# Kernel tuning notes

Measured on AMD Instinct MI355X. Metric: run time of the kernel, lower is better.

The kernel has to match this reference:

```python
import jax, jax.numpy as jnp
import numpy as np

B, H, N, D = 2, 16, 2048, 128

def setup_inputs() -> dict:
    key = jax.random.key(0)
    kq, kk, kv = jax.random.split(key, 3)
    q = jax.random.normal(kq, (B, H, N, D), dtype=jnp.float32)
    k = jax.random.normal(kk, (B, H, N, D), dtype=jnp.float32)
    v = jax.random.normal(kv, (B, H, N, D), dtype=jnp.float32)
    return {"q": q, "k": k, "v": v}

def reference(q, k, v):
    # scale = 1/sqrt(d) computed at forward time (scale=None in __init__)
    d = q.shape[-1]
    scale = 1.0 / jnp.sqrt(jnp.asarray(d, dtype=q.dtype))
    # scores: (B, H, N, N)
    scores = jnp.einsum('bhnd,bhmd->bhnm', q, k) * scale
    probs = jax.nn.softmax(scores, axis=-1)
    return jnp.einsum('bhnm,bhmd->bhnd', probs, v)
```

## Files before the change

kernel.cpp:

```cpp
#include <hip/hip_runtime.h>
#include <hip/hip_bf16.h>
#include <stdint.h>

#define BATCH 2
#define HEADS 16
#define BH    32
#define SEQ   2048
#define DIM   128
#define ELEMS (BATCH*HEADS*SEQ*DIM)

#define KVB   64
#define NT    (SEQ/KVB)

using f32x4  = __attribute__((ext_vector_type(4))) float;
using f32x16 = __attribute__((ext_vector_type(16))) float;
using bf16x8 = __attribute__((ext_vector_type(8))) short;
using us4    = __attribute__((ext_vector_type(4))) unsigned short;

__device__ __forceinline__ unsigned short f2bf(float f) {
    union { float f; uint32_t u; } v; v.f = f;
    uint32_t u = v.u;
    uint32_t r = u + 0x7FFFu + ((u >> 16) & 1u);
    return (unsigned short)(r >> 16);
}

__device__ __forceinline__ uint32_t packbf2(float lo, float hi) {
    __hip_bfloat162 h2 = __float22bfloat162_rn(make_float2(lo, hi));
    union { __hip_bfloat162 h; uint32_t u; } c; c.h = h2;
    return c.u;
}

__global__ __launch_bounds__(256) void prep(const float* __restrict__ K,
                                            const float* __restrict__ V,
                                            unsigned short* __restrict__ kb,
                                            unsigned short* __restrict__ vt) {
    const int b = blockIdx.x, t = threadIdx.x;
    if (b < 2048) {
        size_t base = (size_t)b * 4096 + t * 4;
        #pragma unroll
        for (int j = 0; j < 4; ++j) {
            f32x4 v = *(const f32x4*)(K + base + j * 1024);
            us4 o;
            #pragma unroll
            for (int jj = 0; jj < 4; ++jj) o[jj] = f2bf(v[jj]);
            *(us4*)(kb + base + j * 1024) = o;
        }
    } else {
        __shared__ unsigned short tile[64][66];
        const int b2 = b - 2048;
        const int bh = b2 >> 6, rem = b2 & 63;
        const int n0 = (rem >> 1) * 64, d0 = (rem & 1) * 64;
        const int rr = t >> 4, cc = t & 15;
        #pragma unroll
        for (int j = 0; j < 4; ++j) {
            int row = rr + 16 * j;
            f32x4 v = *(const f32x4*)(V + ((size_t)bh * SEQ + n0 + row) * DIM + d0 + cc * 4);
            #pragma unroll
            for (int jj = 0; jj < 4; ++jj) tile[row][cc * 4 + jj] = f2bf(v[jj]);
        }
        __syncthreads();
        #pragma unroll
        for (int j = 0; j < 4; ++j) {
            int drow = rr + 16 * j;
            us4 o;
            #pragma unroll
            for (int jj = 0; jj < 4; ++jj) o[jj] = tile[cc * 4 + jj][drow];
            *(us4*)(vt + ((size_t)bh * DIM + d0 + drow) * SEQ + n0 + cc * 4) = o;
        }
    }
}

__global__ __launch_bounds__(256, 2) void attn_fwd(const float* __restrict__ Qf,
                                                   const unsigned short* __restrict__ Kb,
                                                   const unsigned short* __restrict__ VTb,
                                                   float* __restrict__ Out) {
    __shared__ __attribute__((aligned(16))) char smem[65536];

    const int head = blockIdx.y;
    const int wid  = threadIdx.x >> 6;
    const int lane = threadIdx.x & 63;
    const int l31  = lane & 31;
    const int hL   = lane >> 5;
    const int q0   = blockIdx.x * 128 + wid * 32;

    const char* KhB  = (const char*)(Kb  + (size_t)head * SEQ * DIM);
    const char* VThB = (const char*)(VTb + (size_t)head * DIM * SEQ);

    const float scl = 0.08838834764831845f * 1.4426950408889634f;
    bf16x8 qf[8];
    {
        const float* qrow = Qf + ((size_t)head * SEQ + q0 + l31) * DIM + 8 * hL;
        #pragma unroll
        for (int u = 0; u < 8; ++u) {
            f32x4 a = *(const f32x4*)(qrow + 16 * u);
            f32x4 b = *(const f32x4*)(qrow + 16 * u + 4);
            union { uint32_t w[4]; bf16x8 v; } P;
            P.w[0] = packbf2(a[0] * scl, a[1] * scl);
            P.w[1] = packbf2(a[2] * scl, a[3] * scl);
            P.w[2] = packbf2(b[0] * scl, b[1] * scl);
            P.w[3] = packbf2(b[2] * scl, b[3] * scl);
            qf[u] = P.v;
        }
    }

    f32x16 acc[4];
    #pragma unroll
    for (int m = 0; m < 4; ++m) acc[m] = (f32x16)(0.f);
    float m_run = -INFINITY, l_run = 0.f;

    const int swzK = (l31 & 15) << 4;
    const int swzV = ((l31 >> 1) & 7) << 4;

    auto STAGE = [&](int buf, int kv0) {
        #pragma unroll
        for (int i = 0; i < 4; ++i) {
            int seg = wid * 4 + i;
            int r   = seg * 4 + (lane >> 4);
            int cb  = ((lane & 15) << 4) ^ ((r & 15) << 4);
            const char* g = KhB + (((size_t)(kv0 + r)) << 8) + cb;
            __builtin_amdgcn_global_load_lds(
                (const __attribute__((address_space(1))) void*)g,
                (__attribute__((address_space(3))) void*)(smem + buf * 16384 + seg * 1024),
                16, 0, 0);
        }
        #pragma unroll
        for (int i = 0; i < 4; ++i) {
            int seg = wid * 4 + i;
            int rp  = seg * 4 + (lane >> 4);
            int q8  = (lane & 15) << 4;
            int pre = q8 ^ ((rp & 7) << 4);
            int r   = 2 * rp + (pre >> 7);
            int cb  = pre & 127;
            const char* g = VThB + (size_t)r * (SEQ * 2) + ((size_t)kv0 << 1) + cb;
            __builtin_amdgcn_global_load_lds(
                (const __attribute__((address_space(1))) void*)g,
                (__attribute__((address_space(3))) void*)(smem + 32768 + buf * 16384 + seg * 1024),
                16, 0, 0);
        }
    };

    STAGE(0, 0);

    for (int t = 0; t < NT; ++t) {
        const int cur = t & 1;
        if (t + 1 < NT) {
            STAGE(cur ^ 1, (t + 1) * KVB);
            asm volatile("s_waitcnt vmcnt(8)" ::: "memory");
        } else {
            asm volatile("s_waitcnt vmcnt(0)" ::: "memory");
        }
        __builtin_amdgcn_s_barrier();
        asm volatile("" ::: "memory");

        const char* kb = smem + cur * 16384;
        const char* vb = smem + 32768 + cur * 16384;

        f32x16 s0 = (f32x16)(0.f), s1 = (f32x16)(0.f);
        __builtin_amdgcn_s_setprio(1);
        {
            const char* krow0 = kb + (size_t)l31 * 256;
            const char* krow1 = kb + (size_t)(32 + l31) * 256;
            #pragma unroll
            for (int u = 0; u < 8; ++u) {
                int cb = (32 * u + 16 * hL) ^ swzK;
                bf16x8 k0 = *(const bf16x8*)(krow0 + cb);
                bf16x8 k1 = *(const bf16x8*)(krow1 + cb);
                s0 = __builtin_amdgcn_mfma_f32_32x32x16_bf16(k0, qf[u], s0, 0, 0, 0);
                s1 = __builtin_amdgcn_mfma_f32_32x32x16_bf16(k1, qf[u], s1, 0, 0, 0);
            }
        }
        __builtin_amdgcn_s_setprio(0);

        bf16x8 vf[2][2][4];
        #pragma unroll
        for (int tt = 0; tt < 2; ++tt)
            #pragma unroll
            for (int ssi = 0; ssi < 2; ++ssi) {
                const int cbv = (32 * (2 * tt + ssi) + 16 * hL) + ((l31 & 1) << 7);
                #pragma unroll
                for (int m = 0; m < 4; ++m) {
                    int rp = 16 * m + (l31 >> 1);
                    vf[tt][ssi][m] = *(const bf16x8*)(vb + (size_t)rp * 256 + (cbv ^ swzV));
                }
            }

        float smax = -1e30f;
        #pragma unroll
        for (int r = 0; r < 16; ++r)
            smax = fmaxf(smax, fmaxf(s0[r], s1[r]));
        smax = fmaxf(smax, __shfl_xor(smax, 16) * 0.f + __shfl_xor(smax, 32));
        if (!__all(smax - m_run <= 8.f)) {
            float mnew = fmaxf(m_run, smax);
            float corr = __builtin_amdgcn_exp2f(m_run - mnew);
            #pragma unroll
            for (int m = 0; m < 4; ++m) acc[m] *= corr;
            l_run *= corr;
            m_run = mnew;
        }

        float psum = 0.f;
        #pragma unroll
        for (int r = 0; r < 16; ++r) {
            s0[r] = __builtin_amdgcn_exp2f(s0[r] - m_run);
            s1[r] = __builtin_amdgcn_exp2f(s1[r] - m_run);
            psum += s0[r] + s1[r];
        }
        l_run += psum;

        uint32_t w0[8], w1[8];
        #pragma unroll
        for (int k2 = 0; k2 < 8; ++k2) {
            w0[k2] = packbf2(s0[2 * k2], s0[2 * k2 + 1]);
            w1[k2] = packbf2(s1[2 * k2], s1[2 * k2 + 1]);
        }

        __builtin_amdgcn_s_setprio(1);
        #pragma unroll
        for (int tt = 0; tt < 2; ++tt) {
            #pragma unroll
            for (int ssi = 0; ssi < 2; ++ssi) {
                uint32_t A0 = tt ? w1[4 * ssi]     : w0[4 * ssi];
                uint32_t A1 = tt ? w1[4 * ssi + 1] : w0[4 * ssi + 1];
                uint32_t C0 = tt ? w1[4 * ssi + 2] : w0[4 * ssi + 2];
                uint32_t C1 = tt ? w1[4 * ssi + 3] : w0[4 * ssi + 3];
                uint32_t o0 = hL ? A0 : C0;
                uint32_t o1 = hL ? A1 : C1;
                uint32_t e0 = (uint32_t)__shfl_xor((int)o0, 32);
                uint32_t e1 = (uint32_t)__shfl_xor((int)o1, 32);
                union { uint32_t u[4]; bf16x8 v; } Bf;
                Bf.u[0] = hL ? e0 : A0;
                Bf.u[1] = hL ? e1 : A1;
                Bf.u[2] = hL ? C0 : e0;
                Bf.u[3] = hL ? C1 : e1;
                #pragma unroll
                for (int m = 0; m < 4; ++m)
                    acc[m] = __builtin_amdgcn_mfma_f32_32x32x16_bf16(vf[tt][ssi][m], Bf.v, acc[m], 0, 0, 0);
            }
        }
        __builtin_amdgcn_s_setprio(0);

        asm volatile("" ::: "memory");
        __builtin_amdgcn_s_barrier();
    }

    __syncthreads();
    const float l_tot = l_run + __shfl_xor(l_run, 32);
    const float inv = 1.0f / l_tot;
    float* ob = (float*)(smem + wid * 16384);
    #pragma unroll
    for (int m = 0; m < 4; ++m) {
        #pragma unroll
        for (int r = 0; r < 16; ++r) {
            int d = 32 * m + (r & 3) + 8 * (r >> 2) + 4 * hL;
            ob[l31 * 128 + (d ^ ((l31 & 7) << 2))] = acc[m][r] * inv;
        }
    }
    __syncthreads();
    {
        float* outp = Out + ((size_t)head * SEQ + q0) * DIM;
        #pragma unroll
        for (int i = 0; i < 16; ++i) {
            int row = 2 * i + hL;
            f32x4 v = *(const f32x4*)(ob + row * 128 + ((4 * l31) ^ ((row & 7) << 2)));
            *(f32x4*)(outp + (size_t)row * DIM + 4 * l31) = v;
        }
    }
}

extern "C" void kernel_launch(void* const* d_in, const int* in_sizes, int n_in,
                              void* d_out, int out_size, void* d_ws, size_t ws_size,
                              hipStream_t stream) {
    (void)in_sizes; (void)n_in; (void)out_size;
    const float* q = (const float*)d_in[0];
    const float* k = (const float*)d_in[1];
    const float* v = (const float*)d_in[2];
    float* out = (float*)d_out;

    const size_t needed = (size_t)ELEMS * 2 * 2;
    if (ws_size < needed) return;

    unsigned short* kb = (unsigned short*)d_ws;
    unsigned short* vt = kb + ELEMS;

    prep<<<4096, 256, 0, stream>>>(k, v, kb, vt);
    attn_fwd<<<dim3(SEQ / 128, BH), 256, 0, stream>>>(q, kb, vt, out);
}
```

Measured before the change: 220.0 us.

## Pre-convert scaled Q to bf16 in prep kernel and load V fragments lazily

Q scaling and bf16 conversion move out of the attention kernel into the prep kernel, so attn_fwd loads bf16 Q directly and prep launches 2048 more blocks. V fragment LDS loads move from a batch before the softmax to right before each PV MFMA, which lowers register pressure but may expose LDS latency. A redundant shuffle in the row-max reduction is also dropped. The extra Q write and re-read through global memory adds traffic in exchange for less fp32 Q traffic in the main kernel.

```diff
diff --git a/kernel.cpp b/kernel.cpp
--- a/kernel.cpp
+++ b/kernel.cpp
@@ -30,24 +30,31 @@
     return c.u;
 }
 
-__global__ __launch_bounds__(256) void prep(const float* __restrict__ K,
+__global__ __launch_bounds__(256) void prep(const float* __restrict__ Q,
+                                            const float* __restrict__ K,
                                             const float* __restrict__ V,
+                                            unsigned short* __restrict__ qb,
                                             unsigned short* __restrict__ kb,
                                             unsigned short* __restrict__ vt) {
     const int b = blockIdx.x, t = threadIdx.x;
-    if (b < 2048) {
-        size_t base = (size_t)b * 4096 + t * 4;
+    const float scl = 0.08838834764831845f * 1.4426950408889634f;
+    if (b < 4096) {
+        const bool isQ = b < 2048;
+        const float* src = isQ ? Q : K;
+        unsigned short* dst = isQ ? qb : kb;
+        const float f = isQ ? scl : 1.0f;
+        size_t base = (size_t)(isQ ? b : b - 2048) * 4096 + t * 4;
         #pragma unroll
         for (int j = 0; j < 4; ++j) {
-            f32x4 v = *(const f32x4*)(K + base + j * 1024);
+            f32x4 v = *(const f32x4*)(src + base + j * 1024);
             us4 o;
             #pragma unroll
-            for (int jj = 0; jj < 4; ++jj) o[jj] = f2bf(v[jj]);
-            *(us4*)(kb + base + j * 1024) = o;
+            for (int jj = 0; jj < 4; ++jj) o[jj] = f2bf(v[jj] * f);
+            *(us4*)(dst + base + j * 1024) = o;
         }
     } else {
         __shared__ unsigned short tile[64][66];
-        const int b2 = b - 2048;
+        const int b2 = b - 4096;
         const int bh = b2 >> 6, rem = b2 & 63;
         const int n0 = (rem >> 1) * 64, d0 = (rem & 1) * 64;
         const int rr = t >> 4, cc = t & 15;
@@ -70,7 +77,7 @@
     }
 }
 
-__global__ __launch_bounds__(256, 2) void attn_fwd(const float* __restrict__ Qf,
+__global__ __launch_bounds__(256, 2) void attn_fwd(const unsigned short* __restrict__ Qb,
                                                    const unsigned short* __restrict__ Kb,
                                                    const unsigned short* __restrict__ VTb,
                                                    float* __restrict__ Out) {
@@ -83,24 +90,15 @@
     const int hL   = lane >> 5;
     const int q0   = blockIdx.x * 128 + wid * 32;
 
+    const unsigned short* Qh = Qb + (size_t)head * SEQ * DIM;
     const char* KhB  = (const char*)(Kb  + (size_t)head * SEQ * DIM);
     const char* VThB = (const char*)(VTb + (size_t)head * DIM * SEQ);
 
-    const float scl = 0.08838834764831845f * 1.4426950408889634f;
     bf16x8 qf[8];
     {
-        const float* qrow = Qf + ((size_t)head * SEQ + q0 + l31) * DIM + 8 * hL;
-        #pragma unroll
-        for (int u = 0; u < 8; ++u) {
-            f32x4 a = *(const f32x4*)(qrow + 16 * u);
-            f32x4 b = *(const f32x4*)(qrow + 16 * u + 4);
-            union { uint32_t w[4]; bf16x8 v; } P;
-            P.w[0] = packbf2(a[0] * scl, a[1] * scl);
-            P.w[1] = packbf2(a[2] * scl, a[3] * scl);
-            P.w[2] = packbf2(b[0] * scl, b[1] * scl);
-            P.w[3] = packbf2(b[2] * scl, b[3] * scl);
-            qf[u] = P.v;
-        }
+        const char* qrow = (const char*)(Qh + (size_t)(q0 + l31) * DIM) + 16 * hL;
+        #pragma unroll
+        for (int u = 0; u < 8; ++u) qf[u] = *(const bf16x8*)(qrow + 32 * u);
     }
 
     f32x16 acc[4];
@@ -171,24 +169,12 @@
         }
         __builtin_amdgcn_s_setprio(0);
 
-        bf16x8 vf[2][2][4];
-        #pragma unroll
-        for (int tt = 0; tt < 2; ++tt)
-            #pragma unroll
-            for (int ssi = 0; ssi < 2; ++ssi) {
-                const int cbv = (32 * (2 * tt + ssi) + 16 * hL) + ((l31 & 1) << 7);
-                #pragma unroll
-                for (int m = 0; m < 4; ++m) {
-                    int rp = 16 * m + (l31 >> 1);
-                    vf[tt][ssi][m] = *(const bf16x8*)(vb + (size_t)rp * 256 + (cbv ^ swzV));
-                }
-            }
-
         float smax = -1e30f;
         #pragma unroll
         for (int r = 0; r < 16; ++r)
             smax = fmaxf(smax, fmaxf(s0[r], s1[r]));
-        smax = fmaxf(smax, __shfl_xor(smax, 16) * 0.f + __shfl_xor(smax, 32));
+        smax = fmaxf(smax, __shfl_xor(smax, 32));
+
         if (!__all(smax - m_run <= 8.f)) {
             float mnew = fmaxf(m_run, smax);
             float corr = __builtin_amdgcn_exp2f(m_run - mnew);
@@ -232,9 +218,13 @@
                 Bf.u[1] = hL ? e1 : A1;
                 Bf.u[2] = hL ? C0 : e0;
                 Bf.u[3] = hL ? C1 : e1;
+                const int cbv = (32 * (2 * tt + ssi) + 16 * hL) + ((l31 & 1) << 7);
                 #pragma unroll
-                for (int m = 0; m < 4; ++m)
-                    acc[m] = __builtin_amdgcn_mfma_f32_32x32x16_bf16(vf[tt][ssi][m], Bf.v, acc[m], 0, 0, 0);
+                for (int m = 0; m < 4; ++m) {
+                    int rp = 16 * m + (l31 >> 1);
+                    bf16x8 vf = *(const bf16x8*)(vb + (size_t)rp * 256 + (cbv ^ swzV));
+                    acc[m] = __builtin_amdgcn_mfma_f32_32x32x16_bf16(vf, Bf.v, acc[m], 0, 0, 0);
+                }
             }
         }
         __builtin_amdgcn_s_setprio(0);
@@ -276,12 +266,13 @@
     const float* v = (const float*)d_in[2];
     float* out = (float*)d_out;
 
-    const size_t needed = (size_t)ELEMS * 2 * 2;
+    const size_t needed = (size_t)ELEMS * 2 * 3;
     if (ws_size < needed) return;
 
-    unsigned short* kb = (unsigned short*)d_ws;
+    unsigned short* qb = (unsigned short*)d_ws;
+    unsigned short* kb = qb + ELEMS;
     unsigned short* vt = kb + ELEMS;
 
-    prep<<<4096, 256, 0, stream>>>(k, v, kb, vt);
-    attn_fwd<<<dim3(SEQ / 128, BH), 256, 0, stream>>>(q, kb, vt, out);
-}
+    prep<<<6144, 256, 0, stream>>>(q, k, v, qb, kb, vt);
+    attn_fwd<<<dim3(SEQ / 128, BH), 256, 0, stream>>>(qb, kb, vt, out);
+}
```

Result: no change. 223.8 us (+1.7%).
